# Kernel optimization log

Hardware: AMD Instinct MI355X
Metric: run time of the kernel (lower is better)

The kernel has to match this reference:

```python
import jax, jax.numpy as jnp
import numpy as np

N, B, DIN = 128, 2, 128
D, DFF, NHEAD, NLAYERS = 256, 1024, 8, 2
BLOCK = 32
LENGTH = 160


def setup_inputs() -> dict:
    key = jax.random.key(0)
    ks = jax.random.split(key, 10)
    r = lambda k, sh: jax.random.normal(k, sh, jnp.float32) * 0.05
    return {
        "inputs": jax.random.normal(ks[0], (N, B, DIN), jnp.float32),
        "in_W1": r(ks[1], (DIN, DFF)), "in_b1": jnp.zeros((DFF,), jnp.float32),
        "in_W2": r(ks[2], (DFF, D)), "in_b2": jnp.zeros((D,), jnp.float32),
        "k_W1": r(ks[3], (DIN, DFF)), "k_b1": jnp.zeros((DFF,), jnp.float32),
        "k_W2": r(ks[4], (DFF, 2)), "k_b2": jnp.zeros((2,), jnp.float32),
        "Wqkv": r(ks[5], (NLAYERS, D, 3 * D)), "bqkv": jnp.zeros((NLAYERS, 3 * D), jnp.float32),
        "Wo": r(ks[6], (NLAYERS, D, D)), "bo": jnp.zeros((NLAYERS, D), jnp.float32),
        "ln1_g": jnp.ones((NLAYERS, D), jnp.float32), "ln1_b": jnp.zeros((NLAYERS, D), jnp.float32),
        "W1": r(ks[7], (NLAYERS, D, DFF)), "b1": jnp.zeros((NLAYERS, DFF), jnp.float32),
        "W2": r(ks[8], (NLAYERS, DFF, D)), "b2": jnp.zeros((NLAYERS, D), jnp.float32),
        "ln2_g": jnp.ones((NLAYERS, D), jnp.float32), "ln2_b": jnp.zeros((NLAYERS, D), jnp.float32),
        "length": LENGTH,
    }


def _ln(x, g, b):
    m = jnp.mean(x, axis=-1, keepdims=True)
    v = jnp.mean(jnp.square(x - m), axis=-1, keepdims=True)
    return (x - m) * jax.lax.rsqrt(v + 1e-5) * g + b


def _forward(inputs, in_W1, in_b1, in_W2, in_b2, k_W1, k_b1, k_W2, k_b2,
             Wqkv, bqkv, Wo, bo, ln1_g, ln1_b, W1, b1, W2, b2, ln2_g, ln2_b, length):
    n, b, din = inputs.shape
    d = in_W2.shape[1]
    H, dh = NHEAD, in_W2.shape[1] // NHEAD
    Wmax = 2 * BLOCK + 1
    L = length
    idx = jnp.arange(n)
    starts = jnp.maximum(0, idx - BLOCK)                 # [N]
    ends = jnp.minimum(L, idx + BLOCK + 1)               # [N]
    cols = starts[:, None] + jnp.arange(Wmax)[None, :]   # [N,Wmax] absolute column per window slot
    valid = cols < ends[:, None]                          # [N,Wmax] ragged-window mask

    # sinusoidal PE at absolute column positions (start_idx = max(0, i-block))
    pos = cols.astype(jnp.float32)
    div = jnp.exp(jnp.arange(0, din, 2, dtype=jnp.float32) * (-np.log(10000.0) / din))
    ang = pos[..., None] * div                            # [N,Wmax,din/2]
    pe = jnp.stack([jnp.sin(ang), jnp.cos(ang)], axis=-1).reshape(n, Wmax, din)

    # row token repeated across its window + PE, then input_ff
    x = inputs[:, None, :, :] + pe[:, :, None, :]         # [N,Wmax,B,din]
    h = jnp.maximum(x @ in_W1 + in_b1, 0.0) @ in_W2 + in_b2  # [N,Wmax,B,D]

    # TransformerEncoder (post-norm, relu, eval mode) over the window axis, padded slots masked as keys
    kmask = valid[:, None, None, None, :]                 # [N,1,1,1,Wmax]
    scale = 1.0 / np.sqrt(dh)
    for l in range(Wqkv.shape[0]):
        qkv = h @ Wqkv[l] + bqkv[l]
        q, k, v = [t.reshape(n, Wmax, b, H, dh) for t in jnp.split(qkv, 3, axis=-1)]
        s = jnp.einsum('nqbhe,nkbhe->nbhqk', q, k) * scale
        s = jnp.where(kmask, s, -jnp.inf)
        a = jax.nn.softmax(s, axis=-1)
        o = jnp.einsum('nbhqk,nkbhe->nqbhe', a, v).reshape(n, Wmax, b, d)
        h = _ln(h + o @ Wo[l] + bo[l], ln1_g[l], ln1_b[l])
        f = jnp.maximum(h @ W1[l] + b1[l], 0.0) @ W2[l] + b2[l]
        h = _ln(h + f, ln2_g[l], ln2_b[l])

    # hierarchy kernel scores (Gaussian band kernel with learned (mu, logsig) per row/batch)
    kp = jnp.maximum(inputs @ k_W1 + k_b1, 0.0) @ k_W2 + k_b2   # [N,B,2]
    hscale = L / n
    diff = cols.astype(jnp.float32) - idx[:, None].astype(jnp.float32) * hscale  # [N,Wmax]
    hier = -jnp.square(diff[:, :, None] - kp[:, None, :, 0]) * jnp.exp(kp[:, None, :, 1])  # [N,Wmax,B]

    # scatter banded values/scores into dense [N,L,...] then row-softmax and weighted combine
    n_idx = jnp.broadcast_to(idx[:, None], (n, Wmax))
    scat = jnp.where(valid, cols, L)                      # out-of-bounds -> dropped
    v_mat = jnp.zeros((n, L, b, d), jnp.float32).at[n_idx, scat].set(h, mode='drop')
    h_mat = jnp.full((n, L, b), -jnp.inf, jnp.float32).at[n_idx, scat].set(hier, mode='drop')
    w = jax.nn.softmax(h_mat, axis=0)[..., None]          # softmax over rows per column
    return jnp.sum(v_mat * w, axis=0)                     # [L,B,D]


def reference(inputs, in_W1, in_b1, in_W2, in_b2, k_W1, k_b1, k_W2, k_b2,
              Wqkv, bqkv, Wo, bo, ln1_g, ln1_b, W1, b1, W2, b2, ln2_g, ln2_b, length):
    return _forward(inputs, in_W1, in_b1, in_W2, in_b2, k_W1, k_b1, k_W2, k_b2,
                    Wqkv, bqkv, Wo, bo, ln1_g, ln1_b, W1, b1, W2, b2, ln2_g, ln2_b, length)
```

## Files before the change

kernel.cpp:

```cpp
#include <hip/hip_runtime.h>

constexpr int NN    = 128;
constexpr int BB    = 2;
constexpr int DIN   = 128;
constexpr int DD    = 256;
constexpr int DFF   = 1024;
constexpr int NH    = 8;
constexpr int DH    = 32;
constexpr int NL    = 2;
constexpr int BLK   = 32;
constexpr int WMAX  = 2 * BLK + 1;
constexpr int RROWS = NN * WMAX * BB;

typedef __attribute__((ext_vector_type(8))) short s16x8;
typedef __attribute__((ext_vector_type(4))) float f32x4;

__device__ __forceinline__ ushort f2bf(float f) {
  unsigned u = __float_as_uint(f);
  unsigned r = (u + 0x7fffu + ((u >> 16) & 1u)) >> 16;
  return (ushort)r;
}
__device__ __forceinline__ float bf2f(ushort h) {
  return __uint_as_float(((unsigned)h) << 16);
}
__device__ __forceinline__ float bfl(unsigned u) { return __uint_as_float(u << 16); }
__device__ __forceinline__ float bfh(unsigned u) { return __uint_as_float(u & 0xffff0000u); }

__device__ __forceinline__ void gld16(const void* g, void* l) {
  __builtin_amdgcn_global_load_lds(
      (const __attribute__((address_space(1))) void*)g,
      (__attribute__((address_space(3))) void*)l, 16, 0, 0);
}

struct TD { const float* in; ushort* out; int K; int N; };
struct TPack { TD d[10]; };

__global__ __launch_bounds__(256) void k_wconv(TPack p) {
  TD t = p.d[blockIdx.y];
  int ntk = t.K >> 5, ntn = t.N >> 5;
  int tile = blockIdx.x;
  if (tile >= ntk * ntn) return;
  int tn = tile / ntk, tk = tile - tn * ntk;
  __shared__ float ls[32 * 33];
  int tid = threadIdx.x;
  int r = tid >> 5, c = tid & 31;
#pragma unroll
  for (int i = 0; i < 4; ++i) {
    int kk = r + 8 * i;
    ls[kk * 33 + c] = t.in[(size_t)(tk * 32 + kk) * t.N + tn * 32 + c];
  }
  __syncthreads();
#pragma unroll
  for (int i = 0; i < 4; ++i) {
    int rr = r + 8 * i;
    t.out[(size_t)(tn * 32 + rr) * t.K + tk * 32 + c] = f2bf(ls[c * 33 + rr]);
  }
}

__global__ __launch_bounds__(256) void k_buildx(const float* __restrict__ inp,
                                                ushort* __restrict__ x) {
  int e = blockIdx.x * 256 + threadIdx.x;
  int i = e & 127, r = e >> 7;
  int n = r / (WMAX * BB);
  int rem = r - n * (WMAX * BB);
  int w = rem >> 1, b = rem & 1;
  int st = n - BLK; if (st < 0) st = 0;
  float pos = (float)(st + w);
  float div = __expf(-0.0719557841f * (float)(i & 126));
  float ang = pos * div;
  float pe = (i & 1) ? __cosf(ang) : __sinf(ang);
  x[e] = f2bf(inp[(n * BB + b) * DIN + i] + pe);
}

__global__ __launch_bounds__(256) void k_kp(
    const float* __restrict__ inp, const float* __restrict__ kW1,
    const float* __restrict__ kb1, const float* __restrict__ kW2,
    const float* __restrict__ kb2, float* __restrict__ kp) {
  __shared__ float xs[DIN];
  __shared__ float red[8];
  int row = blockIdx.x;
  int tid = threadIdx.x;
  if (tid < DIN) xs[tid] = inp[row * DIN + tid];
  __syncthreads();
  float a0 = 0.f, a1 = 0.f;
  for (int j = tid; j < DFF; j += 256) {
    float acc = kb1[j];
    for (int k = 0; k < DIN; ++k) acc += xs[k] * kW1[k * DFF + j];
    acc = fmaxf(acc, 0.f);
    a0 += acc * kW2[2 * j];
    a1 += acc * kW2[2 * j + 1];
  }
#pragma unroll
  for (int m = 32; m > 0; m >>= 1) {
    a0 += __shfl_xor(a0, m, 64);
    a1 += __shfl_xor(a1, m, 64);
  }
  if ((tid & 63) == 0) { red[(tid >> 6) * 2] = a0; red[(tid >> 6) * 2 + 1] = a1; }
  __syncthreads();
  if (tid == 0) {
    kp[row * 2 + 0] = red[0] + red[2] + red[4] + red[6] + kb2[0];
    kp[row * 2 + 1] = red[1] + red[3] + red[5] + red[7] + kb2[1];
  }
}

template<int BMT, int RELU, int FUSE_LN>
__global__ __launch_bounds__(512) void k_gemm8(
    const ushort* __restrict__ A, const ushort* __restrict__ Bt,
    const float* __restrict__ bias, const ushort* __restrict__ resid,
    const float* __restrict__ lng, const float* __restrict__ lnb,
    ushort* __restrict__ out, int N, int K) {
  constexpr int MF = BMT / 32;
  __shared__ __align__(16) char As[BMT * 128];
  __shared__ __align__(16) char Bs[256 * 128];
  __shared__ float psum[FUSE_LN ? 4 : 1][FUSE_LN ? BMT : 1];
  __shared__ float psq [FUSE_LN ? 4 : 1][FUSE_LN ? BMT : 1];
  int tid = threadIdx.x;
  int m0 = blockIdx.x * BMT, n0 = blockIdx.y * 256;
  int lane = tid & 63, w = tid >> 6;
  int wr = w >> 2, wc = w & 3;
  int fr = lane & 15, g = lane >> 4;
  f32x4 acc[MF][4] = {};

  for (int kb = 0; kb < K; kb += 64) {
    __syncthreads();
#pragma unroll
    for (int it = 0; it < BMT / 64; ++it) {
      int e = tid + it * 512;
      int row = e >> 3, c = e & 7;
      gld16(A + (size_t)(m0 + row) * K + kb + ((c ^ (row & 7)) * 8), As + e * 16);
    }
#pragma unroll
    for (int it = 0; it < 4; ++it) {
      int e = tid + it * 512;
      int row = e >> 3, c = e & 7;
      gld16(Bt + (size_t)(n0 + row) * K + kb + ((c ^ (row & 7)) * 8), Bs + e * 16);
    }
    __syncthreads();
#pragma unroll
    for (int ks = 0; ks < 2; ++ks) {
      int kByte = ks * 64 + g * 16;
      s16x8 a[MF], b[4];
#pragma unroll
      for (int m = 0; m < MF; ++m) {
        int row = wr * (BMT / 2) + m * 16 + fr;
        a[m] = *(const s16x8*)(As + ((row * 128 + kByte) ^ ((row & 7) << 4)));
      }
#pragma unroll
      for (int n = 0; n < 4; ++n) {
        int row = wc * 64 + n * 16 + fr;
        b[n] = *(const s16x8*)(Bs + ((row * 128 + kByte) ^ ((row & 7) << 4)));
      }
#pragma unroll
      for (int m = 0; m < MF; ++m)
#pragma unroll
        for (int n = 0; n < 4; ++n)
          acc[m][n] = __builtin_amdgcn_mfma_f32_16x16x32_bf16(a[m], b[n], acc[m][n], 0, 0, 0);
    }
  }

  if constexpr (!FUSE_LN) {
#pragma unroll
    for (int m = 0; m < MF; ++m) {
      int rowb = m0 + wr * (BMT / 2) + m * 16 + g * 4;
#pragma unroll
      for (int n = 0; n < 4; ++n) {
        int col = n0 + wc * 64 + n * 16 + fr;
        float bv = bias[col];
#pragma unroll
        for (int j = 0; j < 4; ++j) {
          float v = acc[m][n][j] + bv;
          if (RELU) v = fmaxf(v, 0.f);
          out[(size_t)(rowb + j) * N + col] = f2bf(v);
        }
      }
    }
  } else {
#pragma unroll
    for (int m = 0; m < MF; ++m) {
      int rowb = wr * (BMT / 2) + m * 16 + g * 4;
#pragma unroll
      for (int j = 0; j < 4; ++j) {
        float ps = 0.f, pq = 0.f;
#pragma unroll
        for (int n = 0; n < 4; ++n) {
          int col = wc * 64 + n * 16 + fr;
          float v = acc[m][n][j] + bias[col]
                  + bf2f(resid[(size_t)(m0 + rowb + j) * 256 + col]);
          acc[m][n][j] = v;
          ps += v; pq += v * v;
        }
#pragma unroll
        for (int d = 1; d < 16; d <<= 1) {
          ps += __shfl_xor(ps, d, 64);
          pq += __shfl_xor(pq, d, 64);
        }
        if (fr == 0) { psum[wc][rowb + j] = ps; psq[wc][rowb + j] = pq; }
      }
    }
    __syncthreads();
#pragma unroll
    for (int m = 0; m < MF; ++m) {
      int rowb = wr * (BMT / 2) + m * 16 + g * 4;
#pragma unroll
      for (int j = 0; j < 4; ++j) {
        int lr = rowb + j;
        float sm = psum[0][lr] + psum[1][lr] + psum[2][lr] + psum[3][lr];
        float sq = psq[0][lr] + psq[1][lr] + psq[2][lr] + psq[3][lr];
        float mean = sm * (1.f / 256.f);
        float var = sq * (1.f / 256.f) - mean * mean;
        float rs = rsqrtf(var + 1e-5f);
#pragma unroll
        for (int n = 0; n < 4; ++n) {
          int col = wc * 64 + n * 16 + fr;
          float v = (acc[m][n][j] - mean) * rs * lng[col] + lnb[col];
          out[(size_t)(m0 + lr) * 256 + col] = f2bf(v);
        }
      }
    }
  }
}

constexpr int QKS = 40;
constexpr int VTS = 104;
constexpr int PS  = 104;

__device__ __forceinline__ int vslot(int d, int r) {
  int rc = r >> 3;
  int sw = (rc < 8) ? (rc ^ (d >> 3)) : rc;
  return d * VTS + sw * 8 + (r & 7);
}

__global__ __launch_bounds__(320) void k_attn(
    const ushort* __restrict__ qkv, ushort* __restrict__ o,
    const int* __restrict__ lenp) {
  __shared__ __align__(16) ushort Qs[80 * QKS];
  __shared__ __align__(16) ushort Ks[80 * QKS];
  __shared__ __align__(16) ushort Vt[32 * VTS];
  __shared__ __align__(16) ushort Pb[5 * 16 * PS];
  int L = lenp[0];
  int blk = blockIdx.x;
  int hh = blk & 7;
  int nb = blk >> 3;
  int b = nb & 1;
  int n = nb >> 1;
  int s0 = n - BLK; if (s0 < 0) s0 = 0;
  int e0 = n + BLK + 1; if (e0 > L) e0 = L;
  int vn = e0 - s0;
  int tid = threadIdx.x;

  for (int i = tid; i < 32 * VTS / 2; i += 320) ((uint*)Vt)[i] = 0;
  for (int i = tid; i < 15 * QKS / 2; i += 320) {
    ((uint*)(Qs + 65 * QKS))[i] = 0;
    ((uint*)(Ks + 65 * QKS))[i] = 0;
  }
  for (int e = tid; e < 65 * 4; e += 320) {
    int r = e >> 2, c = e & 3;
    const ushort* base = qkv + ((size_t)(n * WMAX + r) * BB + b) * (3 * DD) + hh * DH;
    *(uint4*)(Qs + r * QKS + c * 8) = *(const uint4*)(base + c * 8);
    *(uint4*)(Ks + r * QKS + c * 8) = *(const uint4*)(base + DD + c * 8);
    uint4 vv = *(const uint4*)(base + 2 * DD + c * 8);
    const ushort* vp = (const ushort*)&vv;
#pragma unroll
    for (int u = 0; u < 8; ++u) Vt[vslot(c * 8 + u, r)] = vp[u];
  }
  __syncthreads();

  int w = tid >> 6, lane = tid & 63;
  int fr = lane & 15, g = lane >> 4;
  int q0 = w * 16;
  ushort* Pw = Pb + w * 16 * PS;

  s16x8 aq = *(const s16x8*)(Qs + (q0 + fr) * QKS + g * 8);
  f32x4 sacc[5];
#pragma unroll
  for (int t = 0; t < 5; ++t) {
    s16x8 bk = *(const s16x8*)(Ks + (t * 16 + fr) * QKS + g * 8);
    f32x4 z = {0.f, 0.f, 0.f, 0.f};
    sacc[t] = __builtin_amdgcn_mfma_f32_16x16x32_bf16(aq, bk, z, 0, 0, 0);
  }
  const float scl = 0.17677669529663687f;
#pragma unroll
  for (int j = 0; j < 4; ++j) {
    float pv[5];
    float mx = -3e38f;
#pragma unroll
    for (int t = 0; t < 5; ++t) {
      bool ok = (t * 16 + fr) < vn;
      pv[t] = ok ? sacc[t][j] * scl : -3e38f;
      mx = fmaxf(mx, pv[t]);
    }
#pragma unroll
    for (int d = 1; d < 16; d <<= 1) mx = fmaxf(mx, __shfl_xor(mx, d, 64));
    float sum = 0.f;
#pragma unroll
    for (int t = 0; t < 5; ++t) {
      float e = ((t * 16 + fr) < vn) ? __expf(pv[t] - mx) : 0.f;
      pv[t] = e;
      sum += e;
    }
#pragma unroll
    for (int d = 1; d < 16; d <<= 1) sum += __shfl_xor(sum, d, 64);
    float inv = 1.f / sum;
#pragma unroll
    for (int t = 0; t < 5; ++t)
      Pw[(g * 4 + j) * PS + t * 16 + fr] = f2bf(pv[t] * inv);
  }
  {
    int zr = lane >> 2, zc = 80 + (lane & 3) * 4;
    *(uint2*)(Pw + zr * PS + zc) = make_uint2(0u, 0u);
  }
  __syncthreads();

  f32x4 oacc[2] = {};
#pragma unroll
  for (int k0 = 0; k0 < 3; ++k0) {
    s16x8 ap = *(const s16x8*)(Pw + fr * PS + k0 * 32 + g * 8);
#pragma unroll
    for (int nt = 0; nt < 2; ++nt) {
      s16x8 bv = *(const s16x8*)(Vt + vslot(nt * 16 + fr, k0 * 32 + g * 8));
      oacc[nt] = __builtin_amdgcn_mfma_f32_16x16x32_bf16(ap, bv, oacc[nt], 0, 0, 0);
    }
  }
#pragma unroll
  for (int nt = 0; nt < 2; ++nt) {
#pragma unroll
    for (int j = 0; j < 4; ++j) {
      int qr = q0 + g * 4 + j;
      if (qr < WMAX)
        o[((size_t)(n * WMAX + qr) * BB + b) * DD + hh * DH + nt * 16 + fr] =
            f2bf(oacc[nt][j]);
    }
  }
}

__global__ __launch_bounds__(256) void k_final(
    const ushort* __restrict__ h, const float* __restrict__ kp,
    float* __restrict__ out, const int* __restrict__ lenp) {
  int L = lenp[0];
  int t = blockIdx.x >> 1, b = blockIdx.x & 1;
  float hsc = (float)L / (float)NN;
  int nlo = t - BLK; if (nlo < 0) nlo = 0;
  int nhi = t + BLK; if (nhi > NN - 1) nhi = NN - 1;
  float mx = -3e38f;
  for (int n = nlo; n <= nhi; ++n) {
    float kp0 = kp[(n * BB + b) * 2 + 0];
    float kp1 = kp[(n * BB + b) * 2 + 1];
    float dif = (float)t - (float)n * hsc - kp0;
    float lg = -dif * dif * __expf(kp1);
    mx = fmaxf(mx, lg);
  }
  float sum = 0.f, acc = 0.f;
  int c = threadIdx.x;
  for (int n = nlo; n <= nhi; ++n) {
    float kp0 = kp[(n * BB + b) * 2 + 0];
    float kp1 = kp[(n * BB + b) * 2 + 1];
    float dif = (float)t - (float)n * hsc - kp0;
    float lg = -dif * dif * __expf(kp1);
    float p = __expf(lg - mx);
    sum += p;
    int st = n - BLK; if (st < 0) st = 0;
    int w = t - st;
    acc += p * bf2f(h[(size_t)((n * WMAX + w) * BB + b) * DD + c]);
  }
  out[(size_t)(t * BB + b) * DD + c] = acc / sum;
}

extern "C" void kernel_launch(void* const* d_in, const int* in_sizes, int n_in,
                              void* d_out, int out_size, void* d_ws, size_t ws_size,
                              hipStream_t stream) {
  const float* inputs = (const float*)d_in[0];
  const float* in_W1  = (const float*)d_in[1];
  const float* in_b1  = (const float*)d_in[2];
  const float* in_W2  = (const float*)d_in[3];
  const float* in_b2  = (const float*)d_in[4];
  const float* k_W1   = (const float*)d_in[5];
  const float* k_b1   = (const float*)d_in[6];
  const float* k_W2   = (const float*)d_in[7];
  const float* k_b2   = (const float*)d_in[8];
  const float* Wqkv   = (const float*)d_in[9];
  const float* bqkv   = (const float*)d_in[10];
  const float* Wo     = (const float*)d_in[11];
  const float* bo     = (const float*)d_in[12];
  const float* ln1_g  = (const float*)d_in[13];
  const float* ln1_b  = (const float*)d_in[14];
  const float* W1     = (const float*)d_in[15];
  const float* b1     = (const float*)d_in[16];
  const float* W2     = (const float*)d_in[17];
  const float* b2     = (const float*)d_in[18];
  const float* ln2_g  = (const float*)d_in[19];
  const float* ln2_b  = (const float*)d_in[20];
  const int*   lenp   = (const int*)d_in[21];
  float* out = (float*)d_out;
  (void)in_sizes; (void)n_in; (void)ws_size;

  ushort* wsu = (ushort*)d_ws;
  size_t off = 0;
  auto alloc = [&](size_t nelem) { ushort* p = wsu + off; off += (nelem + 7) & ~7ull; return p; };
  ushort* inW1t = alloc((size_t)DFF * DIN);
  ushort* inW2t = alloc((size_t)DD * DFF);
  ushort* Wqkvt = alloc((size_t)NL * 3 * DD * DD);
  ushort* Wot   = alloc((size_t)NL * DD * DD);
  ushort* W1t   = alloc((size_t)NL * DFF * DD);
  ushort* W2t   = alloc((size_t)NL * DD * DFF);
  ushort* x     = alloc((size_t)RROWS * DIN);
  ushort* tq    = alloc((size_t)RROWS * DFF);
  ushort* hb    = alloc((size_t)RROWS * DD);
  ushort* ob    = alloc((size_t)RROWS * DD);
  float*  kp    = (float*)(wsu + off);

  int L = out_size / (BB * DD);

  TPack tp;
  tp.d[0] = {in_W1, inW1t, DIN, DFF};
  tp.d[1] = {in_W2, inW2t, DFF, DD};
  tp.d[2] = {Wqkv,                        Wqkvt,                       DD, 3 * DD};
  tp.d[3] = {Wqkv + (size_t)DD * 3 * DD,  Wqkvt + (size_t)3 * DD * DD, DD, 3 * DD};
  tp.d[4] = {Wo,                    Wot,                   DD, DD};
  tp.d[5] = {Wo + (size_t)DD * DD,  Wot + (size_t)DD * DD, DD, DD};
  tp.d[6] = {W1,                      W1t,                    DD, DFF};
  tp.d[7] = {W1 + (size_t)DD * DFF,   W1t + (size_t)DFF * DD, DD, DFF};
  tp.d[8] = {W2,                      W2t,                    DFF, DD};
  tp.d[9] = {W2 + (size_t)DFF * DD,   W2t + (size_t)DD * DFF, DFF, DD};
  k_wconv<<<dim3(256, 10), 256, 0, stream>>>(tp);

  k_buildx<<<RROWS * DIN / 256, 256, 0, stream>>>(inputs, x);
  k_kp<<<NN * BB, 256, 0, stream>>>(inputs, k_W1, k_b1, k_W2, k_b2, kp);

  k_gemm8<128, 1, 0><<<dim3(RROWS / 128, 4), 512, 0, stream>>>(
      x, inW1t, in_b1, nullptr, nullptr, nullptr, tq, DFF, DIN);
  k_gemm8<64, 0, 0><<<dim3(RROWS / 64, 1), 512, 0, stream>>>(
      tq, inW2t, in_b2, nullptr, nullptr, nullptr, hb, DD, DFF);

  for (int l = 0; l < NL; ++l) {
    k_gemm8<128, 0, 0><<<dim3(RROWS / 128, 3), 512, 0, stream>>>(
        hb, Wqkvt + (size_t)l * 3 * DD * DD, bqkv + (size_t)l * 3 * DD,
        nullptr, nullptr, nullptr, tq, 3 * DD, DD);
    k_attn<<<NN * BB * NH, 320, 0, stream>>>(tq, ob, lenp);
    k_gemm8<64, 0, 1><<<dim3(RROWS / 64, 1), 512, 0, stream>>>(
        ob, Wot + (size_t)l * DD * DD, bo + (size_t)l * DD, hb,
        ln1_g + (size_t)l * DD, ln1_b + (size_t)l * DD, hb, DD, DD);
    k_gemm8<128, 1, 0><<<dim3(RROWS / 128, 4), 512, 0, stream>>>(
        hb, W1t + (size_t)l * DFF * DD, b1 + (size_t)l * DFF,
        nullptr, nullptr, nullptr, tq, DFF, DD);
    k_gemm8<64, 0, 1><<<dim3(RROWS / 64, 1), 512, 0, stream>>>(
        tq, W2t + (size_t)l * DD * DFF, b2 + (size_t)l * DD, hb,
        ln2_g + (size_t)l * DD, ln2_b + (size_t)l * DD, hb, DD, DFF);
  }
  k_final<<<L * BB, 256, 0, stream>>>(hb, kp, out, lenp);
}
```

Before: 285.6 us.

## Fuse prep kernels, double-buffer narrow GEMMs, and load attention Q from global

Merges the weight conversion, input/positional-encoding build and kernel-parameter MLP into one launch to save launch overhead and idle time between small kernels. Adds an optional double-buffered LDS pipeline to the BMT=64 GEMMs (in_W2, Wo+LN, W2+LN), overlapping global-to-LDS loads with MFMA work. The LN partial sums now reuse the A tile buffer instead of separate shared arrays. Attention loads Q fragments straight from global memory instead of staging them in LDS, which lowers LDS use but makes the per-lane loads less coalesced.

Result: faster. 268.1 us (-6.1%).

```diff
diff --git a/kernel.cpp b/kernel.cpp
--- a/kernel.cpp
+++ b/kernel.cpp
@@ -31,89 +31,94 @@
       (const __attribute__((address_space(1))) void*)g,
       (__attribute__((address_space(3))) void*)l, 16, 0, 0);
 }
+__device__ __forceinline__ void vmdrain() {
+  asm volatile("s_waitcnt vmcnt(0)" ::: "memory");
+}
 
 struct TD { const float* in; ushort* out; int K; int N; };
 struct TPack { TD d[10]; };
-
-__global__ __launch_bounds__(256) void k_wconv(TPack p) {
-  TD t = p.d[blockIdx.y];
-  int ntk = t.K >> 5, ntn = t.N >> 5;
-  int tile = blockIdx.x;
-  if (tile >= ntk * ntn) return;
-  int tn = tile / ntk, tk = tile - tn * ntk;
+constexpr int WCONV_TILES = 1920;
+constexpr int BX_BLOCKS   = RROWS * DIN / 256;
+
+__global__ __launch_bounds__(256) void k_prep(
+    TPack p, const float* __restrict__ inp, ushort* __restrict__ x,
+    const float* __restrict__ kW1, const float* __restrict__ kb1,
+    const float* __restrict__ kW2, const float* __restrict__ kb2,
+    float* __restrict__ kp) {
   __shared__ float ls[32 * 33];
+  int bid = blockIdx.x;
   int tid = threadIdx.x;
-  int r = tid >> 5, c = tid & 31;
-#pragma unroll
-  for (int i = 0; i < 4; ++i) {
-    int kk = r + 8 * i;
-    ls[kk * 33 + c] = t.in[(size_t)(tk * 32 + kk) * t.N + tn * 32 + c];
-  }
-  __syncthreads();
-#pragma unroll
-  for (int i = 0; i < 4; ++i) {
-    int rr = r + 8 * i;
-    t.out[(size_t)(tn * 32 + rr) * t.K + tk * 32 + c] = f2bf(ls[c * 33 + rr]);
-  }
-}
-
-__global__ __launch_bounds__(256) void k_buildx(const float* __restrict__ inp,
-                                                ushort* __restrict__ x) {
-  int e = blockIdx.x * 256 + threadIdx.x;
-  int i = e & 127, r = e >> 7;
-  int n = r / (WMAX * BB);
-  int rem = r - n * (WMAX * BB);
-  int w = rem >> 1, b = rem & 1;
-  int st = n - BLK; if (st < 0) st = 0;
-  float pos = (float)(st + w);
-  float div = __expf(-0.0719557841f * (float)(i & 126));
-  float ang = pos * div;
-  float pe = (i & 1) ? __cosf(ang) : __sinf(ang);
-  x[e] = f2bf(inp[(n * BB + b) * DIN + i] + pe);
-}
-
-__global__ __launch_bounds__(256) void k_kp(
-    const float* __restrict__ inp, const float* __restrict__ kW1,
-    const float* __restrict__ kb1, const float* __restrict__ kW2,
-    const float* __restrict__ kb2, float* __restrict__ kp) {
-  __shared__ float xs[DIN];
-  __shared__ float red[8];
-  int row = blockIdx.x;
-  int tid = threadIdx.x;
-  if (tid < DIN) xs[tid] = inp[row * DIN + tid];
-  __syncthreads();
-  float a0 = 0.f, a1 = 0.f;
-  for (int j = tid; j < DFF; j += 256) {
-    float acc = kb1[j];
-    for (int k = 0; k < DIN; ++k) acc += xs[k] * kW1[k * DFF + j];
-    acc = fmaxf(acc, 0.f);
-    a0 += acc * kW2[2 * j];
-    a1 += acc * kW2[2 * j + 1];
-  }
-#pragma unroll
-  for (int m = 32; m > 0; m >>= 1) {
-    a0 += __shfl_xor(a0, m, 64);
-    a1 += __shfl_xor(a1, m, 64);
-  }
-  if ((tid & 63) == 0) { red[(tid >> 6) * 2] = a0; red[(tid >> 6) * 2 + 1] = a1; }
-  __syncthreads();
-  if (tid == 0) {
-    kp[row * 2 + 0] = red[0] + red[2] + red[4] + red[6] + kb2[0];
-    kp[row * 2 + 1] = red[1] + red[3] + red[5] + red[7] + kb2[1];
-  }
-}
-
-template<int BMT, int RELU, int FUSE_LN>
+  if (bid < WCONV_TILES) {
+    const int cum[11] = {0, 128, 384, 576, 768, 832, 896, 1152, 1408, 1664, 1920};
+    int mi = 0;
+#pragma unroll
+    for (int i = 0; i < 10; ++i) if (bid >= cum[i + 1]) mi = i + 1;
+    TD t = p.d[mi];
+    int tile = bid - cum[mi];
+    int ntk = t.K >> 5;
+    int tn = tile / ntk, tk = tile - tn * ntk;
+    int r = tid >> 5, c = tid & 31;
+#pragma unroll
+    for (int i = 0; i < 4; ++i) {
+      int kk = r + 8 * i;
+      ls[kk * 33 + c] = t.in[(size_t)(tk * 32 + kk) * t.N + tn * 32 + c];
+    }
+    __syncthreads();
+#pragma unroll
+    for (int i = 0; i < 4; ++i) {
+      int rr = r + 8 * i;
+      t.out[(size_t)(tn * 32 + rr) * t.K + tk * 32 + c] = f2bf(ls[c * 33 + rr]);
+    }
+  } else if (bid < WCONV_TILES + BX_BLOCKS) {
+    int e = (bid - WCONV_TILES) * 256 + tid;
+    int i = e & 127, r = e >> 7;
+    int n = r / (WMAX * BB);
+    int rem = r - n * (WMAX * BB);
+    int w = rem >> 1, b = rem & 1;
+    int st = n - BLK; if (st < 0) st = 0;
+    float pos = (float)(st + w);
+    float div = __expf(-0.0719557841f * (float)(i & 126));
+    float ang = pos * div;
+    float pe = (i & 1) ? __cosf(ang) : __sinf(ang);
+    x[e] = f2bf(inp[(n * BB + b) * DIN + i] + pe);
+  } else {
+    int row = bid - (WCONV_TILES + BX_BLOCKS);
+    float* xs = ls;
+    float* red = ls + 256;
+    if (tid < DIN) xs[tid] = inp[row * DIN + tid];
+    __syncthreads();
+    float a0 = 0.f, a1 = 0.f;
+    for (int j = tid; j < DFF; j += 256) {
+      float acc = kb1[j];
+      for (int k = 0; k < DIN; ++k) acc += xs[k] * kW1[k * DFF + j];
+      acc = fmaxf(acc, 0.f);
+      a0 += acc * kW2[2 * j];
+      a1 += acc * kW2[2 * j + 1];
+    }
+#pragma unroll
+    for (int m = 32; m > 0; m >>= 1) {
+      a0 += __shfl_xor(a0, m, 64);
+      a1 += __shfl_xor(a1, m, 64);
+    }
+    if ((tid & 63) == 0) { red[(tid >> 6) * 2] = a0; red[(tid >> 6) * 2 + 1] = a1; }
+    __syncthreads();
+    if (tid == 0) {
+      kp[row * 2 + 0] = red[0] + red[2] + red[4] + red[6] + kb2[0];
+      kp[row * 2 + 1] = red[1] + red[3] + red[5] + red[7] + kb2[1];
+    }
+  }
+}
+
+template<int BMT, int RELU, int FUSE_LN, int DBUF>
 __global__ __launch_bounds__(512) void k_gemm8(
     const ushort* __restrict__ A, const ushort* __restrict__ Bt,
     const float* __restrict__ bias, const ushort* __restrict__ resid,
     const float* __restrict__ lng, const float* __restrict__ lnb,
     ushort* __restrict__ out, int N, int K) {
   constexpr int MF = BMT / 32;
-  __shared__ __align__(16) char As[BMT * 128];
-  __shared__ __align__(16) char Bs[256 * 128];
-  __shared__ float psum[FUSE_LN ? 4 : 1][FUSE_LN ? BMT : 1];
-  __shared__ float psq [FUSE_LN ? 4 : 1][FUSE_LN ? BMT : 1];
+  constexpr int NB = DBUF ? 2 : 1;
+  __shared__ __align__(16) char As[NB * BMT * 128];
+  __shared__ __align__(16) char Bs[NB * 256 * 128];
   int tid = threadIdx.x;
   int m0 = blockIdx.x * BMT, n0 = blockIdx.y * 256;
   int lane = tid & 63, w = tid >> 6;
@@ -121,21 +126,26 @@
   int fr = lane & 15, g = lane >> 4;
   f32x4 acc[MF][4] = {};
 
-  for (int kb = 0; kb < K; kb += 64) {
-    __syncthreads();
+  auto stage = [&](int half, int tk) {
+    int kb = tk * 64;
+    char* Ah = As + half * (BMT * 128);
+    char* Bh = Bs + half * (256 * 128);
 #pragma unroll
     for (int it = 0; it < BMT / 64; ++it) {
       int e = tid + it * 512;
       int row = e >> 3, c = e & 7;
-      gld16(A + (size_t)(m0 + row) * K + kb + ((c ^ (row & 7)) * 8), As + e * 16);
+      gld16(A + (size_t)(m0 + row) * K + kb + ((c ^ (row & 7)) * 8), Ah + e * 16);
     }
 #pragma unroll
     for (int it = 0; it < 4; ++it) {
       int e = tid + it * 512;
       int row = e >> 3, c = e & 7;
-      gld16(Bt + (size_t)(n0 + row) * K + kb + ((c ^ (row & 7)) * 8), Bs + e * 16);
-    }
-    __syncthreads();
+      gld16(Bt + (size_t)(n0 + row) * K + kb + ((c ^ (row & 7)) * 8), Bh + e * 16);
+    }
+  };
+  auto compute = [&](int half) {
+    const char* Ah = As + half * (BMT * 128);
+    const char* Bh = Bs + half * (256 * 128);
 #pragma unroll
     for (int ks = 0; ks < 2; ++ks) {
       int kByte = ks * 64 + g * 16;
@@ -143,18 +153,39 @@
 #pragma unroll
       for (int m = 0; m < MF; ++m) {
         int row = wr * (BMT / 2) + m * 16 + fr;
-        a[m] = *(const s16x8*)(As + ((row * 128 + kByte) ^ ((row & 7) << 4)));
+        a[m] = *(const s16x8*)(Ah + ((row * 128 + kByte) ^ ((row & 7) << 4)));
       }
 #pragma unroll
       for (int n = 0; n < 4; ++n) {
         int row = wc * 64 + n * 16 + fr;
-        b[n] = *(const s16x8*)(Bs + ((row * 128 + kByte) ^ ((row & 7) << 4)));
+        b[n] = *(const s16x8*)(Bh + ((row * 128 + kByte) ^ ((row & 7) << 4)));
       }
 #pragma unroll
       for (int m = 0; m < MF; ++m)
 #pragma unroll
         for (int n = 0; n < 4; ++n)
           acc[m][n] = __builtin_amdgcn_mfma_f32_16x16x32_bf16(a[m], b[n], acc[m][n], 0, 0, 0);
+    }
+  };
+
+  int nt = K >> 6;
+  if constexpr (DBUF) {
+    stage(0, 0);
+    vmdrain();
+    __syncthreads();
+    for (int t = 0; t < nt; ++t) {
+      if (t + 1 < nt) stage((t + 1) & 1, t + 1);
+      compute(t & 1);
+      vmdrain();
+      __syncthreads();
+    }
+  } else {
+    for (int t = 0; t < nt; ++t) {
+      stage(0, t);
+      vmdrain();
+      __syncthreads();
+      compute(0);
+      __syncthreads();
     }
   }
 
@@ -175,6 +206,8 @@
       }
     }
   } else {
+    float* psum = (float*)As;
+    float* psq  = (float*)(As + 4 * BMT * 4);
 #pragma unroll
     for (int m = 0; m < MF; ++m) {
       int rowb = wr * (BMT / 2) + m * 16 + g * 4;
@@ -194,7 +227,7 @@
           ps += __shfl_xor(ps, d, 64);
           pq += __shfl_xor(pq, d, 64);
         }
-        if (fr == 0) { psum[wc][rowb + j] = ps; psq[wc][rowb + j] = pq; }
+        if (fr == 0) { psum[wc * BMT + rowb + j] = ps; psq[wc * BMT + rowb + j] = pq; }
       }
     }
     __syncthreads();
@@ -204,8 +237,8 @@
 #pragma unroll
       for (int j = 0; j < 4; ++j) {
         int lr = rowb + j;
-        float sm = psum[0][lr] + psum[1][lr] + psum[2][lr] + psum[3][lr];
-        float sq = psq[0][lr] + psq[1][lr] + psq[2][lr] + psq[3][lr];
+        float sm = psum[lr] + psum[BMT + lr] + psum[2 * BMT + lr] + psum[3 * BMT + lr];
+        float sq = psq[lr] + psq[BMT + lr] + psq[2 * BMT + lr] + psq[3 * BMT + lr];
         float mean = sm * (1.f / 256.f);
         float var = sq * (1.f / 256.f) - mean * mean;
         float rs = rsqrtf(var + 1e-5f);
@@ -233,7 +266,6 @@
 __global__ __launch_bounds__(320) void k_attn(
     const ushort* __restrict__ qkv, ushort* __restrict__ o,
     const int* __restrict__ lenp) {
-  __shared__ __align__(16) ushort Qs[80 * QKS];
   __shared__ __align__(16) ushort Ks[80 * QKS];
   __shared__ __align__(16) ushort Vt[32 * VTS];
   __shared__ __align__(16) ushort Pb[5 * 16 * PS];
@@ -249,28 +281,29 @@
   int tid = threadIdx.x;
 
   for (int i = tid; i < 32 * VTS / 2; i += 320) ((uint*)Vt)[i] = 0;
-  for (int i = tid; i < 15 * QKS / 2; i += 320) {
-    ((uint*)(Qs + 65 * QKS))[i] = 0;
+  for (int i = tid; i < 15 * QKS / 2; i += 320)
     ((uint*)(Ks + 65 * QKS))[i] = 0;
-  }
+  __syncthreads();
   for (int e = tid; e < 65 * 4; e += 320) {
     int r = e >> 2, c = e & 3;
     const ushort* base = qkv + ((size_t)(n * WMAX + r) * BB + b) * (3 * DD) + hh * DH;
-    *(uint4*)(Qs + r * QKS + c * 8) = *(const uint4*)(base + c * 8);
     *(uint4*)(Ks + r * QKS + c * 8) = *(const uint4*)(base + DD + c * 8);
     uint4 vv = *(const uint4*)(base + 2 * DD + c * 8);
     const ushort* vp = (const ushort*)&vv;
 #pragma unroll
     for (int u = 0; u < 8; ++u) Vt[vslot(c * 8 + u, r)] = vp[u];
   }
-  __syncthreads();
 
   int w = tid >> 6, lane = tid & 63;
   int fr = lane & 15, g = lane >> 4;
   int q0 = w * 16;
   ushort* Pw = Pb + w * 16 * PS;
 
-  s16x8 aq = *(const s16x8*)(Qs + (q0 + fr) * QKS + g * 8);
+  int qr_ld = q0 + fr; if (qr_ld > 64) qr_ld = 64;
+  s16x8 aq = *(const s16x8*)(qkv + ((size_t)(n * WMAX + qr_ld) * BB + b) * (3 * DD)
+                             + hh * DH + g * 8);
+  __syncthreads();
+
   f32x4 sacc[5];
 #pragma unroll
   for (int t = 0; t < 5; ++t) {
@@ -421,28 +454,27 @@
   tp.d[7] = {W1 + (size_t)DD * DFF,   W1t + (size_t)DFF * DD, DD, DFF};
   tp.d[8] = {W2,                      W2t,                    DFF, DD};
   tp.d[9] = {W2 + (size_t)DFF * DD,   W2t + (size_t)DD * DFF, DFF, DD};
-  k_wconv<<<dim3(256, 10), 256, 0, stream>>>(tp);
-
-  k_buildx<<<RROWS * DIN / 256, 256, 0, stream>>>(inputs, x);
-  k_kp<<<NN * BB, 256, 0, stream>>>(inputs, k_W1, k_b1, k_W2, k_b2, kp);
-
-  k_gemm8<128, 1, 0><<<dim3(RROWS / 128, 4), 512, 0, stream>>>(
+
+  k_prep<<<WCONV_TILES + BX_BLOCKS + NN * BB, 256, 0, stream>>>(
+      tp, inputs, x, k_W1, k_b1, k_W2, k_b2, kp);
+
+  k_gemm8<128, 1, 0, 0><<<dim3(RROWS / 128, 4), 512, 0, stream>>>(
       x, inW1t, in_b1, nullptr, nullptr, nullptr, tq, DFF, DIN);
-  k_gemm8<64, 0, 0><<<dim3(RROWS / 64, 1), 512, 0, stream>>>(
+  k_gemm8<64, 0, 0, 1><<<dim3(RROWS / 64, 1), 512, 0, stream>>>(
       tq, inW2t, in_b2, nullptr, nullptr, nullptr, hb, DD, DFF);
 
   for (int l = 0; l < NL; ++l) {
-    k_gemm8<128, 0, 0><<<dim3(RROWS / 128, 3), 512, 0, stream>>>(
+    k_gemm8<128, 0, 0, 0><<<dim3(RROWS / 128, 3), 512, 0, stream>>>(
         hb, Wqkvt + (size_t)l * 3 * DD * DD, bqkv + (size_t)l * 3 * DD,
         nullptr, nullptr, nullptr, tq, 3 * DD, DD);
     k_attn<<<NN * BB * NH, 320, 0, stream>>>(tq, ob, lenp);
-    k_gemm8<64, 0, 1><<<dim3(RROWS / 64, 1), 512, 0, stream>>>(
+    k_gemm8<64, 0, 1, 1><<<dim3(RROWS / 64, 1), 512, 0, stream>>>(
         ob, Wot + (size_t)l * DD * DD, bo + (size_t)l * DD, hb,
         ln1_g + (size_t)l * DD, ln1_b + (size_t)l * DD, hb, DD, DD);
-    k_gemm8<128, 1, 0><<<dim3(RROWS / 128, 4), 512, 0, stream>>>(
+    k_gemm8<128, 1, 0, 0><<<dim3(RROWS / 128, 4), 512, 0, stream>>>(
         hb, W1t + (size_t)l * DFF * DD, b1 + (size_t)l * DFF,
         nullptr, nullptr, nullptr, tq, DFF, DD);
-    k_gemm8<64, 0, 1><<<dim3(RROWS / 64, 1), 512, 0, stream>>>(
+    k_gemm8<64, 0, 1, 1><<<dim3(RROWS / 64, 1), 512, 0, stream>>>(
         tq, W2t + (size_t)l * DD * DFF, b2 + (size_t)l * DD, hb,
         ln2_g + (size_t)l * DD, ln2_b + (size_t)l * DD, hb, DD, DFF);
   }
```
